# Optimization experiments

Measured on AMD Instinct MI355X. Metric: run time of the kernel, lower is better.

Reference implementation:

```python
import jax, jax.numpy as jnp
import numpy as np

T, K, E, H, I = 1024, 2, 8, 2048, 768


def setup_inputs() -> dict:
    key = jax.random.key(0)
    k1, k2, k3, k4, k5 = jax.random.split(key, 5)
    hidden_states = jax.random.normal(k1, (T, H), dtype=jnp.float32)
    top_k_index = jax.random.randint(k2, (T, K), 0, E)
    logits = jax.random.normal(k3, (T, K), dtype=jnp.float32)
    top_k_weights = jax.nn.softmax(logits, axis=-1)  # realistic routing weights
    # Linear-style weights: gate_up [E, 2I, H], down [E, H, I]; scaled like trained params
    gate_up_proj = jax.random.normal(k4, (E, 2 * I, H), dtype=jnp.float32) * 0.02
    down_proj = jax.random.normal(k5, (E, H, I), dtype=jnp.float32) * 0.02
    return {
        "hidden_states": hidden_states,
        "top_k_index": top_k_index,
        "top_k_weights": top_k_weights,
        "gate_up_proj": gate_up_proj,
        "down_proj": down_proj,
    }


def reference(hidden_states, top_k_index, top_k_weights, gate_up_proj, down_proj):
    """Dense-dispatch MoE forward: same math as the per-expert 4-bit loop.

    For every token t and routed expert e (with routing weight w):
      gate, up = split(x_t @ Wgu_e^T); y_t += w * (silu(gate)*up) @ Wd_e^T
    Expressed densely over experts; non-routed (token, expert) pairs get a
    combine weight of 0, so they contribute nothing.
    """
    num_experts = gate_up_proj.shape[0]
    # combine[t, e] = sum_k w[t,k] * [top_k_index[t,k] == e]
    combine = jnp.sum(
        jax.nn.one_hot(top_k_index, num_experts, dtype=hidden_states.dtype)
        * top_k_weights[..., None],
        axis=1,
    )  # [T, E]
    # gate_up: [T, E, 2I]
    gu = jnp.einsum("th,eoh->teo", hidden_states, gate_up_proj)
    gate, up = jnp.split(gu, 2, axis=-1)
    h = jax.nn.silu(gate) * up  # [T, E, I]
    # fold combine weight in before the down projection (scalar per (t,e))
    h = h * combine[:, :, None]
    out = jnp.einsum("tei,ehi->th", h, down_proj)  # [T, H]
    return out.astype(hidden_states.dtype)
```

## Files before the change

kernel.cpp:

```cpp
#include <hip/hip_runtime.h>
#include <hip/hip_bf16.h>

#define T_TOK 1024
#define TOPK  2
#define NEXP  8
#define HDIM  2048
#define IDIM  768
#define MROW  384

typedef __attribute__((ext_vector_type(4))) float f32x4;
typedef __attribute__((ext_vector_type(8))) short bf16x8;
typedef __attribute__((ext_vector_type(8))) unsigned short u16x8;
typedef __attribute__((ext_vector_type(8))) __bf16 bfv8;

__device__ __forceinline__ bf16x8 cvt8(f32x4 v0, f32x4 v1) {
  bfv8 r;
#pragma unroll
  for (int j = 0; j < 4; ++j) { r[j] = (__bf16)v0[j]; r[4 + j] = (__bf16)v1[j]; }
  return __builtin_bit_cast(bf16x8, r);
}

__device__ __forceinline__ void gload_lds16(const void* g, void* l) {
  __builtin_amdgcn_global_load_lds(
      (const __attribute__((address_space(1))) unsigned int*)((unsigned long long)g),
      (__attribute__((address_space(3))) unsigned int*)(unsigned int)(unsigned long long)(l),
      16, 0, 0);
}


__global__ void k_gather(const int* __restrict__ idx, const float* __restrict__ wts,
                         int* __restrict__ cnt, int* __restrict__ tok,
                         float* __restrict__ wl, int* __restrict__ inv) {
  int g = blockIdx.x * 256 + threadIdx.x;
  int e = idx[g];
  float w = wts[g];
  int pos = atomicAdd(&cnt[e], 1);
  if (pos < 2048) { tok[e * 2048 + pos] = g; wl[e * 2048 + pos] = w; }
  inv[g] = (pos < MROW) ? (e * MROW + pos) : -1;
}

__global__ __launch_bounds__(256) void k_compact(const float* __restrict__ x,
                                                 const int* __restrict__ inv,
                                                 unsigned short* __restrict__ xe) {
  int pid = blockIdx.x;
  int iv = inv[pid];
  if (iv < 0) return;
  const float* src = x + (size_t)(pid >> 1) * HDIM;
  unsigned short* dst = xe + (size_t)iv * HDIM;
  int i = threadIdx.x * 8;
  f32x4 a = *(const f32x4*)(src + i);
  f32x4 b = *(const f32x4*)(src + i + 4);
  *(bf16x8*)(dst + i) = cvt8(a, b);
}

__global__ __launch_bounds__(256) void k_gate_up(
    const unsigned short* __restrict__ xe, const float* __restrict__ Wgu,
    const int* __restrict__ cnt, const float* __restrict__ wl,
    unsigned short* __restrict__ hb)
{
  const int b = blockIdx.x;
  const int e = b & 7;
  const int r = b >> 3;
  const int mt = r % 3;
  const int nb = r / 3;
  const int m0 = mt * 128;
  int cc = cnt[e]; if (cc > MROW) cc = MROW;
  if (m0 >= cc) return;
  const int col0 = nb * 32;

  __shared__ unsigned short sA[3 * 4096];
  __shared__ float          sB[3 * 2048];
  __shared__ float sW[128];

  const int tid = threadIdx.x;
  const int lane = tid & 63, wid = tid >> 6;

  if (tid < 128) sW[tid] = (m0 + tid < cc) ? wl[e * 2048 + m0 + tid] : 0.f;

  const unsigned short* xeE = xe + ((size_t)e * MROW + m0) * HDIM;
  const unsigned short* aSrc[2];
  unsigned int aDstOff[2];
#pragma unroll
  for (int i = 0; i < 2; ++i) {
    int row = wid * 32 + i * 16 + (lane >> 2);
    int csrc = (lane & 3) ^ (row & 3);
    aSrc[i] = xeE + (size_t)row * HDIM + csrc * 8;
    aDstOff[i] = (unsigned)(wid * 32 + i * 16) * 32;
  }

  const float* bSrc[2];
  unsigned int bDstOff[2];
#pragma unroll
  for (int i = 0; i < 2; ++i) {
    int row = wid * 16 + i * 8 + (lane >> 3);
    int c = lane & 7, h = c & 1, p = c >> 1;
    int psrc = p ^ (row & 3);
    int ocol = (row < 32) ? (col0 + row) : (IDIM + col0 + (row - 32));
    bSrc[i] = Wgu + ((size_t)e * 2 * IDIM + ocol) * HDIM + psrc * 8 + h * 4;
    bDstOff[i] = (unsigned)(wid * 16 + i * 8) * 32;
  }

  const int fl = lane & 15, q = lane >> 4;
  const int wm = (wid >> 1) * 64, wn = (wid & 1) * 16;

  f32x4 accg[4], accu[4];
#pragma unroll
  for (int rf = 0; rf < 4; ++rf) {
    accg[rf] = f32x4{0.f, 0.f, 0.f, 0.f};
    accu[rf] = f32x4{0.f, 0.f, 0.f, 0.f};
  }

  const int NS = HDIM / 32;

  auto STAGE = [&](int step, int bo) {
    const int kt = step * 32;
#pragma unroll
    for (int i = 0; i < 2; ++i)
      gload_lds16(aSrc[i] + kt, &sA[bo * 4096 + aDstOff[i]]);
#pragma unroll
    for (int i = 0; i < 2; ++i)
      gload_lds16(bSrc[i] + kt, &sB[bo * 2048 + bDstOff[i]]);
  };

  auto COMPUTE = [&](int bo) {
    const unsigned short* A = sA + bo * 4096;
    const float* B = sB + bo * 2048;
    bf16x8 a[4];
#pragma unroll
    for (int rf = 0; rf < 4; ++rf) {
      int rr = wm + rf * 16 + fl;
      a[rf] = *(const bf16x8*)(A + rr * 32 + ((q ^ (rr & 3)) * 8));
    }
    bf16x8 g2, u2;
    {
      int rg = wn + fl;
      const float* pg = B + rg * 32 + ((q ^ (rg & 3)) * 8);
      g2 = cvt8(*(const f32x4*)pg, *(const f32x4*)(pg + 4));
      int ru = 32 + wn + fl;
      const float* pu = B + ru * 32 + ((q ^ (ru & 3)) * 8);
      u2 = cvt8(*(const f32x4*)pu, *(const f32x4*)(pu + 4));
    }
#pragma unroll
    for (int rf = 0; rf < 4; ++rf) {
      accg[rf] = __builtin_amdgcn_mfma_f32_16x16x32_bf16(a[rf], g2, accg[rf], 0, 0, 0);
      accu[rf] = __builtin_amdgcn_mfma_f32_16x16x32_bf16(a[rf], u2, accu[rf], 0, 0, 0);
    }
  };

  STAGE(0, 0);
  STAGE(1, 1);
  asm volatile("s_waitcnt vmcnt(4)" ::: "memory");
  __builtin_amdgcn_sched_barrier(0);
  __builtin_amdgcn_s_barrier();
  __builtin_amdgcn_sched_barrier(0);

  int oC = 0, oN = 1, oNN = 2;
#pragma unroll 1
  for (int i = 0; i < NS; ++i) {
    const bool st = (i + 2) < NS;
    if (st) STAGE(i + 2, oNN);
    COMPUTE(oC);
    if (i < NS - 1) {
      if (st) { asm volatile("s_waitcnt vmcnt(4)" ::: "memory"); }
      else    { asm volatile("s_waitcnt vmcnt(0)" ::: "memory"); }
      __builtin_amdgcn_sched_barrier(0);
      __builtin_amdgcn_s_barrier();
      __builtin_amdgcn_sched_barrier(0);
    }
    int t = oC; oC = oN; oN = oNN; oNN = t;
  }

  unsigned short* hbE = hb + (size_t)e * MROW * IDIM;
  const int q4 = q * 4;
#pragma unroll
  for (int rf = 0; rf < 4; ++rf)
#pragma unroll
    for (int v = 0; v < 4; ++v) {
      int rowl = wm + rf * 16 + q4 + v;
      if (m0 + rowl < cc) {
        float g = accg[rf][v], u = accu[rf][v];
        float s = g / (1.f + __expf(-g));
        float h = s * u * sW[rowl];
        hbE[(size_t)(m0 + rowl) * IDIM + col0 + wn + fl] =
            __builtin_bit_cast(unsigned short, (__bf16)h);
      }
    }
}

__global__ __launch_bounds__(256, 3) void k_down(
    const unsigned short* __restrict__ hb, const float* __restrict__ Wd,
    const int* __restrict__ cnt, const int* __restrict__ tok,
    float* __restrict__ out)
{
  const int b = blockIdx.x;
  const int e = b & 7;
  const int r = b >> 3;
  const int mt = r % 6;
  const int nb = r / 6;
  const int m0 = mt * 64;
  int cc = cnt[e]; if (cc > MROW) cc = MROW;
  if (m0 >= cc) return;
  const int col0 = nb * 64;

  __shared__ unsigned short sA[3 * 4096];
  __shared__ unsigned short sB[3 * 4096];
  __shared__ int sTok[64];

  const int tid = threadIdx.x;
  const int lane = tid & 63, wid = tid >> 6;
  if (tid < 64) sTok[tid] = (m0 + tid < cc) ? (tok[e * 2048 + m0 + tid] >> 1) : 0;

  const unsigned short* hbE = hb + ((size_t)e * MROW + m0) * IDIM;
  const unsigned short* aSrc[2];
  unsigned int aDstOff[2];
#pragma unroll
  for (int i = 0; i < 2; ++i) {
    int row = wid * 16 + i * 8 + (lane >> 3);
    int csrc = (lane & 7) ^ (row & 7);
    aSrc[i] = hbE + (size_t)row * IDIM + csrc * 8;
    aDstOff[i] = (unsigned)(wid * 16 + i * 8) * 64;
  }

  const int brow = tid >> 2, cq = (tid & 3);
  const float* bSrc = Wd + ((size_t)e * HDIM + col0 + brow) * IDIM + cq * 16;
  unsigned int bDst[2];
#pragma unroll
  for (int c2 = 0; c2 < 2; ++c2)
    bDst[c2] = (unsigned)(brow * 64 + (((cq * 2 + c2) ^ (brow & 7)) * 8));

  const int fl = lane & 15, q = lane >> 4;
  const int wm = (wid >> 1) * 32, wn = (wid & 1) * 32;

  f32x4 acc[2][2];
#pragma unroll
  for (int mf = 0; mf < 2; ++mf)
#pragma unroll
    for (int nf = 0; nf < 2; ++nf) acc[mf][nf] = f32x4{0.f, 0.f, 0.f, 0.f};

  f32x4 blA[4], blB[4];
  const int NS = IDIM / 64;

  auto COMPUTE = [&](int bo) {
    const unsigned short* A = sA + bo;
    const unsigned short* B = sB + bo;
#pragma unroll
    for (int s = 0; s < 2; ++s) {
      bf16x8 a[2], bb[2];
#pragma unroll
      for (int mf = 0; mf < 2; ++mf) {
        int rr = wm + mf * 16 + fl;
        a[mf] = *(const bf16x8*)(A + rr * 64 + (((s * 4 + q) ^ (rr & 7)) * 8));
      }
#pragma unroll
      for (int nf = 0; nf < 2; ++nf) {
        int rn = wn + nf * 16 + fl;
        bb[nf] = *(const bf16x8*)(B + rn * 64 + (((s * 4 + q) ^ (rn & 7)) * 8));
      }
#pragma unroll
      for (int mf = 0; mf < 2; ++mf)
#pragma unroll
        for (int nf = 0; nf < 2; ++nf)
          acc[mf][nf] = __builtin_amdgcn_mfma_f32_16x16x32_bf16(a[mf], bb[nf], acc[mf][nf], 0, 0, 0);
    }
  };

  auto ITER = [&](int ks, f32x4 (&blR)[4], f32x4 (&blW)[4],
                  int oC, int oN, int oNN) {
    const bool nL = (ks + 2) < NS;
    const bool nW = (ks + 1) < NS;
    if (nL) {
#pragma unroll
      for (int i = 0; i < 2; ++i)
        gload_lds16(aSrc[i] + (ks + 2) * 64, &sA[oNN + aDstOff[i]]);
#pragma unroll
      for (int j = 0; j < 4; ++j)
        blW[j] = *(const f32x4*)(bSrc + (ks + 2) * 64 + j * 4);
    }
    if (nW) {
#pragma unroll
      for (int c2 = 0; c2 < 2; ++c2)
        *(bf16x8*)&sB[oN + bDst[c2]] = cvt8(blR[c2 * 2], blR[c2 * 2 + 1]);
    }
    COMPUTE(oC);
    if (nW) {
      if (nL) { asm volatile("s_waitcnt vmcnt(6) lgkmcnt(0)" ::: "memory"); }
      else    { asm volatile("s_waitcnt vmcnt(0) lgkmcnt(0)" ::: "memory"); }
      __builtin_amdgcn_sched_barrier(0);
      __builtin_amdgcn_s_barrier();
      __builtin_amdgcn_sched_barrier(0);
    }
  };

#pragma unroll
  for (int i = 0; i < 2; ++i) gload_lds16(aSrc[i], &sA[aDstOff[i]]);
#pragma unroll
  for (int j = 0; j < 4; ++j) blA[j] = *(const f32x4*)(bSrc + j * 4);
#pragma unroll
  for (int i = 0; i < 2; ++i) gload_lds16(aSrc[i] + 64, &sA[4096 + aDstOff[i]]);
#pragma unroll
  for (int j = 0; j < 4; ++j) blB[j] = *(const f32x4*)(bSrc + 64 + j * 4);
#pragma unroll
  for (int c2 = 0; c2 < 2; ++c2)
    *(bf16x8*)&sB[bDst[c2]] = cvt8(blA[c2 * 2], blA[c2 * 2 + 1]);
  asm volatile("s_waitcnt vmcnt(6) lgkmcnt(0)" ::: "memory");
  __builtin_amdgcn_sched_barrier(0);
  __builtin_amdgcn_s_barrier();
  __builtin_amdgcn_sched_barrier(0);

  int oC = 0, oN = 4096, oNN = 8192;
  for (int ks = 0; ks < NS; ks += 2) {
    ITER(ks, blB, blA, oC, oN, oNN);
    int t = oC; oC = oN; oN = oNN; oNN = t;
    ITER(ks + 1, blA, blB, oC, oN, oNN);
    t = oC; oC = oN; oN = oNN; oNN = t;
  }

  const int q4 = q * 4;
#pragma unroll
  for (int mf = 0; mf < 2; ++mf)
#pragma unroll
    for (int nf = 0; nf < 2; ++nf)
#pragma unroll
      for (int v = 0; v < 4; ++v) {
        int rowl = wm + mf * 16 + q4 + v;
        if (m0 + rowl < cc) {
          int t = sTok[rowl];
          atomicAdd(out + (size_t)t * HDIM + col0 + wn + nf * 16 + fl, acc[mf][nf][v]);
        }
      }
}

extern "C" void kernel_launch(void* const* d_in, const int* in_sizes, int n_in,
                              void* d_out, int out_size, void* d_ws, size_t ws_size,
                              hipStream_t stream) {
  const float* x   = (const float*)d_in[0];
  const int*   idx = (const int*)d_in[1];
  const float* wts = (const float*)d_in[2];
  const float* Wgu = (const float*)d_in[3];
  const float* Wd  = (const float*)d_in[4];
  float* out = (float*)d_out;

  char* ws = (char*)d_ws;
  int*            cnt = (int*)(ws + 0);
  int*            tok = (int*)(ws + 64);
  float*          wl  = (float*)(ws + 65600);
  int*            inv = (int*)(ws + 131136);
  unsigned short* xe  = (unsigned short*)(ws + 139328);
  unsigned short* hb  = (unsigned short*)(ws + 12722240);

  hipMemsetAsync(cnt, 0, NEXP * sizeof(int), stream);
  hipMemsetAsync(out, 0, (size_t)T_TOK * HDIM * sizeof(float), stream);
  k_gather<<<dim3((T_TOK * TOPK) / 256), 256, 0, stream>>>(idx, wts, cnt, tok, wl, inv);
  k_compact<<<dim3(T_TOK * TOPK), 256, 0, stream>>>(x, inv, xe);
  k_gate_up<<<dim3(NEXP * 3 * 24), 256, 0, stream>>>(xe, Wgu, cnt, wl, hb);
  k_down<<<dim3(NEXP * 6 * 32), 256, 0, stream>>>(hb, Wd, cnt, tok, out);
}
```

Measured before the change: 105.2 us.

## Split-K the gate/up GEMM into two halves with a separate SiLU epilogue kernel

```diff
diff --git a/kernel.cpp b/kernel.cpp
--- a/kernel.cpp
+++ b/kernel.cpp
@@ -9,6 +9,7 @@
 #define MROW  384
 
 typedef __attribute__((ext_vector_type(4))) float f32x4;
+typedef __attribute__((ext_vector_type(4))) unsigned short u16x4;
 typedef __attribute__((ext_vector_type(8))) short bf16x8;
 typedef __attribute__((ext_vector_type(8))) unsigned short u16x8;
 typedef __attribute__((ext_vector_type(8))) __bf16 bfv8;
@@ -27,6 +28,9 @@
       16, 0, 0);
 }
 
+#define GUP_OFF   17440832ull
+#define GUP_HALF  (8ull * MROW * 1536)
+#define WS_NEEDED (GUP_OFF + 2ull * GUP_HALF * 4ull)
 
 __global__ void k_gather(const int* __restrict__ idx, const float* __restrict__ wts,
                          int* __restrict__ cnt, int* __restrict__ tok,
@@ -51,6 +55,163 @@
   f32x4 a = *(const f32x4*)(src + i);
   f32x4 b = *(const f32x4*)(src + i + 4);
   *(bf16x8*)(dst + i) = cvt8(a, b);
+}
+
+__global__ __launch_bounds__(256) void k_gate_up_ks(
+    const unsigned short* __restrict__ xe, const float* __restrict__ Wgu,
+    const int* __restrict__ cnt, float* __restrict__ guP)
+{
+  const int b = blockIdx.x;
+  const int e = b & 7;
+  const int r = b >> 3;
+  const int ks = r & 1;
+  const int r2 = r >> 1;
+  const int mt = r2 % 3;
+  const int nb = r2 / 3;
+  const int m0 = mt * 128;
+  int cc = cnt[e]; if (cc > MROW) cc = MROW;
+  if (m0 >= cc) return;
+  const int col0 = nb * 32;
+  const int kbase = ks * (HDIM / 2);
+
+  __shared__ unsigned short sA[3 * 4096];
+  __shared__ float          sB[3 * 2048];
+
+  const int tid = threadIdx.x;
+  const int lane = tid & 63, wid = tid >> 6;
+
+  const unsigned short* xeE = xe + ((size_t)e * MROW + m0) * HDIM + kbase;
+  const unsigned short* aSrc[2];
+  unsigned int aDstOff[2];
+#pragma unroll
+  for (int i = 0; i < 2; ++i) {
+    int row = wid * 32 + i * 16 + (lane >> 2);
+    int csrc = (lane & 3) ^ (row & 3);
+    aSrc[i] = xeE + (size_t)row * HDIM + csrc * 8;
+    aDstOff[i] = (unsigned)(wid * 32 + i * 16) * 32;
+  }
+
+  const float* bSrc[2];
+  unsigned int bDstOff[2];
+#pragma unroll
+  for (int i = 0; i < 2; ++i) {
+    int row = wid * 16 + i * 8 + (lane >> 3);
+    int c = lane & 7, h = c & 1, p = c >> 1;
+    int psrc = p ^ (row & 3);
+    int ocol = (row < 32) ? (col0 + row) : (IDIM + col0 + (row - 32));
+    bSrc[i] = Wgu + ((size_t)e * 2 * IDIM + ocol) * HDIM + kbase + psrc * 8 + h * 4;
+    bDstOff[i] = (unsigned)(wid * 16 + i * 8) * 32;
+  }
+
+  const int fl = lane & 15, q = lane >> 4;
+  const int wm = (wid >> 1) * 64, wn = (wid & 1) * 16;
+
+  f32x4 accg[4], accu[4];
+#pragma unroll
+  for (int rf = 0; rf < 4; ++rf) {
+    accg[rf] = f32x4{0.f, 0.f, 0.f, 0.f};
+    accu[rf] = f32x4{0.f, 0.f, 0.f, 0.f};
+  }
+
+  const int NS = (HDIM / 2) / 32;
+
+  auto STAGE = [&](int step, int bo) {
+    const int kt = step * 32;
+#pragma unroll
+    for (int i = 0; i < 2; ++i)
+      gload_lds16(aSrc[i] + kt, &sA[bo * 4096 + aDstOff[i]]);
+#pragma unroll
+    for (int i = 0; i < 2; ++i)
+      gload_lds16(bSrc[i] + kt, &sB[bo * 2048 + bDstOff[i]]);
+  };
+
+  auto COMPUTE = [&](int bo) {
+    const unsigned short* A = sA + bo * 4096;
+    const float* B = sB + bo * 2048;
+    bf16x8 a[4];
+#pragma unroll
+    for (int rf = 0; rf < 4; ++rf) {
+      int rr = wm + rf * 16 + fl;
+      a[rf] = *(const bf16x8*)(A + rr * 32 + ((q ^ (rr & 3)) * 8));
+    }
+    bf16x8 g2, u2;
+    {
+      int rg = wn + fl;
+      const float* pg = B + rg * 32 + ((q ^ (rg & 3)) * 8);
+      g2 = cvt8(*(const f32x4*)pg, *(const f32x4*)(pg + 4));
+      int ru = 32 + wn + fl;
+      const float* pu = B + ru * 32 + ((q ^ (ru & 3)) * 8);
+      u2 = cvt8(*(const f32x4*)pu, *(const f32x4*)(pu + 4));
+    }
+#pragma unroll
+    for (int rf = 0; rf < 4; ++rf) {
+      accg[rf] = __builtin_amdgcn_mfma_f32_16x16x32_bf16(a[rf], g2, accg[rf], 0, 0, 0);
+      accu[rf] = __builtin_amdgcn_mfma_f32_16x16x32_bf16(a[rf], u2, accu[rf], 0, 0, 0);
+    }
+  };
+
+  STAGE(0, 0);
+  STAGE(1, 1);
+  asm volatile("s_waitcnt vmcnt(4)" ::: "memory");
+  __builtin_amdgcn_sched_barrier(0);
+  __builtin_amdgcn_s_barrier();
+  __builtin_amdgcn_sched_barrier(0);
+
+  int oC = 0, oN = 1, oNN = 2;
+#pragma unroll 1
+  for (int i = 0; i < NS; ++i) {
+    const bool st = (i + 2) < NS;
+    if (st) STAGE(i + 2, oNN);
+    COMPUTE(oC);
+    if (i < NS - 1) {
+      if (st) { asm volatile("s_waitcnt vmcnt(4)" ::: "memory"); }
+      else    { asm volatile("s_waitcnt vmcnt(0)" ::: "memory"); }
+      __builtin_amdgcn_sched_barrier(0);
+      __builtin_amdgcn_s_barrier();
+      __builtin_amdgcn_sched_barrier(0);
+    }
+    int t = oC; oC = oN; oN = oNN; oNN = t;
+  }
+
+  float* guE = guP + (size_t)ks * GUP_HALF + ((size_t)e * MROW) * 1536;
+  const int q4 = q * 4;
+#pragma unroll
+  for (int rf = 0; rf < 4; ++rf)
+#pragma unroll
+    for (int v = 0; v < 4; ++v) {
+      int rowl = wm + rf * 16 + q4 + v;
+      if (m0 + rowl < cc) {
+        size_t base = (size_t)(m0 + rowl) * 1536 + col0 + wn + fl;
+        guE[base]       = accg[rf][v];
+        guE[base + 768] = accu[rf][v];
+      }
+    }
+}
+
+__global__ __launch_bounds__(256) void k_silu_ep(
+    const float* __restrict__ guP, const int* __restrict__ cnt,
+    const float* __restrict__ wl, unsigned short* __restrict__ hb)
+{
+  int id = blockIdx.x * 256 + threadIdx.x;
+  int e = id / (MROW * 192);
+  int rem = id % (MROW * 192);
+  int row = rem / 192;
+  int c4 = (rem % 192) * 4;
+  int cc = cnt[e]; if (cc > MROW) cc = MROW;
+  if (row >= cc) return;
+
+  size_t base = ((size_t)e * MROW + row) * 1536 + c4;
+  f32x4 g = *(const f32x4*)(guP + base) + *(const f32x4*)(guP + GUP_HALF + base);
+  f32x4 u = *(const f32x4*)(guP + base + 768) + *(const f32x4*)(guP + GUP_HALF + base + 768);
+  float w = wl[e * 2048 + row];
+
+  u16x4 o;
+#pragma unroll
+  for (int j = 0; j < 4; ++j) {
+    float s = g[j] / (1.f + __expf(-g[j]));
+    o[j] = __builtin_bit_cast(unsigned short, (__bf16)(s * u[j] * w));
+  }
+  *(u16x4*)(hb + ((size_t)e * MROW + row) * IDIM + c4) = o;
 }
 
 __global__ __launch_bounds__(256) void k_gate_up(
@@ -347,11 +508,18 @@
   int*            inv = (int*)(ws + 131136);
   unsigned short* xe  = (unsigned short*)(ws + 139328);
   unsigned short* hb  = (unsigned short*)(ws + 12722240);
+  float*          guP = (float*)(ws + GUP_OFF);
 
   hipMemsetAsync(cnt, 0, NEXP * sizeof(int), stream);
   hipMemsetAsync(out, 0, (size_t)T_TOK * HDIM * sizeof(float), stream);
   k_gather<<<dim3((T_TOK * TOPK) / 256), 256, 0, stream>>>(idx, wts, cnt, tok, wl, inv);
   k_compact<<<dim3(T_TOK * TOPK), 256, 0, stream>>>(x, inv, xe);
-  k_gate_up<<<dim3(NEXP * 3 * 24), 256, 0, stream>>>(xe, Wgu, cnt, wl, hb);
+
+  if (ws_size >= WS_NEEDED) {
+    k_gate_up_ks<<<dim3(NEXP * 3 * 24 * 2), 256, 0, stream>>>(xe, Wgu, cnt, guP);
+    k_silu_ep<<<dim3(NEXP * MROW * 192 / 256), 256, 0, stream>>>(guP, cnt, wl, hb);
+  } else {
+    k_gate_up<<<dim3(NEXP * 3 * 24), 256, 0, stream>>>(xe, Wgu, cnt, wl, hb);
+  }
   k_down<<<dim3(NEXP * 6 * 32), 256, 0, stream>>>(hb, Wd, cnt, tok, out);
 }
```

New measurement: 105.5 us. About the same (+0.4%).
